# Kernel optimization log

Hardware: AMD Instinct MI355X
Metric: run time of the kernel (lower is better)

The kernel has to match this reference:

```python
import jax, jax.numpy as jnp
import numpy as np
from jax import lax

B, S, T, H, VIN, VOUT = 32, 128, 64, 512, 32000, 32000
PAD_IDX = 1


def setup_inputs() -> dict:
    key = jax.random.key(0)
    ks = jax.random.split(key, 20)
    sc = 0.05
    rn = lambda k, shp: (jax.random.normal(k, shp, jnp.float32) * sc)
    return {
        "src": jax.random.randint(ks[0], (B, S), 0, VIN),
        "src_len": jnp.full((B,), S, dtype=jnp.int32),
        "trg": jax.random.randint(ks[1], (B, T), 0, VOUT),
        "enc_emb": rn(ks[2], (VIN, H)),
        "enc_wih": rn(ks[3], (4 * H, H)),
        "enc_whh": rn(ks[4], (4 * H, H)),
        "enc_bih": rn(ks[5], (4 * H,)),
        "enc_bhh": rn(ks[6], (4 * H,)),
        "enc_fc_w": rn(ks[7], (H, H)),
        "enc_fc_b": rn(ks[8], (H,)),
        "dec_emb": rn(ks[9], (VOUT, H)),
        "attn_w": rn(ks[10], (H, 2 * H)),
        "attn_b": rn(ks[11], (H,)),
        "attn_v": rn(ks[12], (H,)),
        "dec_wih": rn(ks[13], (4 * H, 2 * H)),
        "dec_whh": rn(ks[14], (4 * H, H)),
        "dec_bih": rn(ks[15], (4 * H,)),
        "dec_bhh": rn(ks[16], (4 * H,)),
        "out_w": rn(ks[17], (VOUT, 3 * H)),
        "out_b": rn(ks[18], (VOUT,)),
    }


def _lstm_cell(x, h, c, wih, whh, bih, bhh):
    # PyTorch gate order: i, f, g, o
    g = x @ wih.T + bih + h @ whh.T + bhh
    i, f, gg, o = jnp.split(g, 4, axis=-1)
    c = jax.nn.sigmoid(f) * c + jax.nn.sigmoid(i) * jnp.tanh(gg)
    h = jax.nn.sigmoid(o) * jnp.tanh(c)
    return h, c


def reference(src, src_len, trg, enc_emb, enc_wih, enc_whh, enc_bih, enc_bhh,
              enc_fc_w, enc_fc_b, dec_emb, attn_w, attn_b, attn_v,
              dec_wih, dec_whh, dec_bih, dec_bhh, out_w, out_b):
    b = src.shape[0]
    # ---- Encoder: single-layer LSTM over time (full lengths) ----
    emb = enc_emb[src].transpose(1, 0, 2)  # [S,B,H] time-major
    h0 = jnp.zeros((b, H), emb.dtype)
    c0 = jnp.zeros((b, H), emb.dtype)

    def enc_step(carry, x_t):
        h, c = carry
        h, c = _lstm_cell(x_t, h, c, enc_wih, enc_whh, enc_bih, enc_bhh)
        return (h, c), h

    (hf, cf), enc_out = lax.scan(enc_step, (h0, c0), emb)  # enc_out [S,B,H]
    hidden = jnp.tanh(hf @ enc_fc_w.T + enc_fc_b)  # [B,H]
    enc_bt = enc_out.transpose(1, 0, 2)  # [B,S,H]
    mask = src != PAD_IDX  # [B,S]

    # ---- Decoder: teacher forcing (ratio=1.0), scan over target steps ----
    def dec_step(carry, tok):
        h, c = carry
        e = dec_emb[tok]  # [B,H]
        # Bahdanau attention
        hrep = jnp.broadcast_to(h[:, None, :], enc_bt.shape)  # [B,S,H]
        energy = jnp.tanh(jnp.concatenate([hrep, enc_bt], -1) @ attn_w.T + attn_b)
        score = energy @ attn_v  # [B,S]
        score = jnp.where(mask, score, jnp.float32(-1e10))
        a = jax.nn.softmax(score, axis=1)
        weighted = jnp.einsum('bs,bsh->bh', a, enc_bt)  # [B,H]
        x = jnp.concatenate([e, weighted], -1)  # [B,2H]
        h, c = _lstm_cell(x, h, c, dec_wih, dec_whh, dec_bih, dec_bhh)
        pred = jnp.concatenate([h, weighted, e], -1) @ out_w.T + out_b  # [B,V]
        return (h, c), pred

    tokens = trg.T  # [T,B]
    (_, _), logits = lax.scan(dec_step, (hidden, cf), tokens[:-1])  # [T-1,B,V]
    outputs = jnp.concatenate(
        [jnp.zeros((1, b, VOUT), logits.dtype), logits], axis=0)  # [T,B,V]
    return outputs
```

## Files before the change

### kernel.cpp

```cpp
#include <hip/hip_runtime.h>

typedef unsigned short u16;
typedef unsigned int u32;
typedef unsigned long long u64;
typedef __attribute__((ext_vector_type(8))) short bf16x8;
typedef __attribute__((ext_vector_type(8))) unsigned short u16x8;
typedef __attribute__((ext_vector_type(4))) unsigned short u16x4;
typedef __attribute__((ext_vector_type(4))) float f32x4;

#define DEVI static __device__ __forceinline__

constexpr int B = 32, S = 128, T = 64, H = 512, V = 32000;
constexpr int H4 = 4 * H;
constexpr int TD = T - 1;
constexpr int MOUT = TD * B;
constexpr int KOUT = 3 * H;
constexpr int PAD_IDX = 1;

DEVI u16 f2bf(float f) {
  union { float f; unsigned u; } v; v.f = f;
  unsigned r = (v.u + 0x7fffu + ((v.u >> 16) & 1u)) >> 16;
  return (u16)r;
}
DEVI float bf2f(u16 h) {
  union { unsigned u; float f; } v; v.u = ((unsigned)h) << 16;
  return v.f;
}
DEVI float sigm(float x) { return 1.f / (1.f + __expf(-x)); }
DEVI float tanh_(float x) {
  float ax = fabsf(x);
  float e = __expf(-2.f * ax);
  float t = (1.f - e) / (1.f + e);
  return x < 0.f ? -t : t;
}
DEVI float tanhf_(float x) {
  float e = __expf(2.f * x);
  return 1.f - 2.f * __builtin_amdgcn_rcpf(e + 1.f);
}
DEVI int swz(int row, int k8) { return row * 32 + ((k8 ^ (row & 3)) << 3); }

DEVI u64 pack4u(const u16* p) {
  return (u64)p[0] | ((u64)p[1] << 16) | ((u64)p[2] << 32) | ((u64)p[3] << 48);
}
DEVI u64 xstore(u16* p, u64 v) {
  return __hip_atomic_exchange((u64*)p, v, __ATOMIC_RELAXED,
                               __HIP_MEMORY_SCOPE_AGENT);
}
DEVI void sstore(unsigned* p, unsigned v) {
  __hip_atomic_exchange(p, v, __ATOMIC_RELAXED, __HIP_MEMORY_SCOPE_AGENT);
}
DEVI void poll_slot(unsigned* p, unsigned tgt) {
  long long t0 = (long long)__builtin_amdgcn_s_memrealtime();
  while (__hip_atomic_load(p, __ATOMIC_RELAXED, __HIP_MEMORY_SCOPE_AGENT) <
         tgt) {
    __builtin_amdgcn_s_sleep(1);
    if ((long long)__builtin_amdgcn_s_memrealtime() - t0 > 20000000ll) break;
  }
}

__global__ __launch_bounds__(256) void gemm_bt(
    const u16* __restrict__ A, int lda,
    const u16* __restrict__ Bt, int ldb,
    float* __restrict__ C, int ldc,
    const float* __restrict__ bias, int M, int K, int bf16out) {
  __shared__ u16 As[128 * 32], Bs[128 * 32];
  const int tid = threadIdx.x;
  const int m0 = blockIdx.y * 128, n0 = blockIdx.x * 128;
  const int lane = tid & 63, w = tid >> 6, wm = w >> 1, wn = w & 1;
  const int lr = lane & 15, lk = lane >> 4;
  f32x4 acc[4][4] = {};
  const int r = tid >> 1, cc = (tid & 1) * 16, k8b = (tid & 1) * 2;

  for (int k0 = 0; k0 < K; k0 += 32) {
    {
      long gr = m0 + r;
      u16x8 v0 = {}, v1 = {};
      if (gr < M) {
        const u16* s = A + gr * (long)lda + k0 + cc;
        v0 = *(const u16x8*)s;
        v1 = *(const u16x8*)(s + 8);
      }
      *(u16x8*)&As[swz(r, k8b)] = v0;
      *(u16x8*)&As[swz(r, k8b + 1)] = v1;
    }
    {
      const u16* s = Bt + (long)(n0 + r) * ldb + k0 + cc;
      u16x8 v0 = *(const u16x8*)s;
      u16x8 v1 = *(const u16x8*)(s + 8);
      *(u16x8*)&Bs[swz(r, k8b)] = v0;
      *(u16x8*)&Bs[swz(r, k8b + 1)] = v1;
    }
    __syncthreads();
    bf16x8 af[4], bfr[4];
#pragma unroll
    for (int mi = 0; mi < 4; mi++)
      af[mi] = *(const bf16x8*)&As[swz(wm * 64 + mi * 16 + lr, lk)];
#pragma unroll
    for (int ni = 0; ni < 4; ni++)
      bfr[ni] = *(const bf16x8*)&Bs[swz(wn * 64 + ni * 16 + lr, lk)];
#pragma unroll
    for (int mi = 0; mi < 4; mi++)
#pragma unroll
      for (int ni = 0; ni < 4; ni++)
        acc[mi][ni] = __builtin_amdgcn_mfma_f32_16x16x32_bf16(
            af[mi], bfr[ni], acc[mi][ni], 0, 0, 0);
    __syncthreads();
  }
#pragma unroll
  for (int ni = 0; ni < 4; ni++) {
    int col = n0 + wn * 64 + ni * 16 + lr;
    float bs = bias ? bias[col] : 0.f;
#pragma unroll
    for (int mi = 0; mi < 4; mi++) {
#pragma unroll
      for (int rr = 0; rr < 4; rr++) {
        long row = m0 + wm * 64 + mi * 16 + lk * 4 + rr;
        if (row < M) {
          float v = acc[mi][ni][rr] + bs;
          if (bf16out)
            ((u16*)C)[row * (long)ldc + col] = f2bf(v);
          else
            C[row * (long)ldc + col] = v;
        }
      }
    }
  }
}

__global__ void zero_f(float* p, long n) {
  long i = (long)blockIdx.x * 256 + threadIdx.x;
  long st = (long)gridDim.x * 256;
  for (; i < n; i += st) p[i] = 0.f;
}

__global__ void zero_u(unsigned* p, int n) {
  int i = blockIdx.x * 256 + threadIdx.x;
  if (i < n) p[i] = 0u;
}

__global__ void cast_bf(const float* __restrict__ src, u16* __restrict__ dst,
                        int ld, int off, int Csz) {
  long row = blockIdx.y;
  int col = blockIdx.x * 256 + threadIdx.x;
  dst[row * Csz + col] = f2bf(src[row * ld + off + col]);
}

__global__ void cast_bf4(const float* __restrict__ src, u16* __restrict__ dst,
                         long n4) {
  long i = (long)blockIdx.x * 256 + threadIdx.x;
  if (i >= n4) return;
  float4 v = ((const float4*)src)[i];
  u16x4 o;
  o[0] = f2bf(v.x); o[1] = f2bf(v.y); o[2] = f2bf(v.z); o[3] = f2bf(v.w);
  *(u16x4*)&dst[i * 4] = o;
}

__global__ void cast_perm(const float* __restrict__ src, int ld, int off,
                          u16* __restrict__ dst) {
  int np = blockIdx.y;
  int c = blockIdx.x * 256 + threadIdx.x;
  int g = np & 3, jH = np >> 2;
  dst[(size_t)np * H + c] = f2bf(src[(size_t)(g * H + jH) * ld + off + c]);
}

__global__ void bias_perm(const float* __restrict__ a,
                          const float* __restrict__ b, float* __restrict__ o) {
  int np = blockIdx.x * 256 + threadIdx.x;
  int g = np & 3, jH = np >> 2;
  int r = g * H + jH;
  o[np] = a[r] + b[r];
}

__global__ __launch_bounds__(256) void cast_transpose_bf(
    const float* __restrict__ src, int ld, int off, u16* __restrict__ dst,
    int R) {
  __shared__ float tile[32][33];
  int r0 = blockIdx.y * 32, c0 = blockIdx.x * 32;
  int tx = threadIdx.x & 31, ty = threadIdx.x >> 5;
#pragma unroll
  for (int i = 0; i < 32; i += 8)
    tile[ty + i][tx] = src[(long)(r0 + ty + i) * ld + off + c0 + tx];
  __syncthreads();
#pragma unroll
  for (int i = 0; i < 32; i += 8)
    dst[(long)(c0 + ty + i) * R + r0 + tx] = f2bf(tile[tx][ty + i]);
}

__global__ void gather_src_emb(const int* __restrict__ src,
                               const float* __restrict__ emb,
                               u16* __restrict__ dst) {
  int row = blockIdx.y;
  int t = row >> 5, b = row & 31;
  int c = blockIdx.x * 256 + threadIdx.x;
  int tok = src[b * S + t];
  dst[(long)row * H + c] = f2bf(emb[(long)tok * H + c]);
}

__global__ void gather_trg_emb(const int* __restrict__ trg,
                               const float* __restrict__ emb,
                               u16* __restrict__ xout) {
  int row = blockIdx.y;
  int t = row >> 5, b = row & 31;
  int c = blockIdx.x * 256 + threadIdx.x;
  int tok = trg[b * T + t];
  xout[(long)row * KOUT + 2 * H + c] = f2bf(emb[(long)tok * H + c]);
}

__global__ __launch_bounds__(128) void enc_persist(
    unsigned* fes, const float* __restrict__ whh,
    const float* __restrict__ xih_p, u16* hstep, u16* enc_bt_bf, float* cbuf) {
  const int tid = threadIdx.x, bk = blockIdx.x;
  const int wave = tid >> 6, lane = tid & 63;
  __shared__ float gs[32][16];
  __shared__ float c_s[128];
  __shared__ u16 hx[128];
  bf16x8 wf[16];
  {
    int n = lane & 15, g = n & 3, q = n >> 2;
    const float* wrow =
        whh + ((size_t)g * H + bk * 4 + q) * H + (lane >> 4) * 8;
#pragma unroll
    for (int kt = 0; kt < 16; kt++) {
      bf16x8 f;
#pragma unroll
      for (int e = 0; e < 8; e++) f[e] = (short)f2bf(wrow[kt * 32 + e]);
      wf[kt] = f;
    }
  }
  c_s[tid] = 0.f;
  for (int t = 0; t < S; t++) {
    if (t > 0) {
      poll_slot(fes + tid * 16, (unsigned)t);
      __syncthreads();
    }
    float4 xv = *(const float4*)(xih_p + ((size_t)t * B + (tid >> 2)) * H4 +
                                 (bk * 4 + (tid & 3)) * 4);
    if (t > 0) {
      const u16* hb = hstep + (size_t)t * B * H +
                      (size_t)(wave * 16 + (lane & 15)) * H + (lane >> 4) * 8;
      f32x4 acc = {};
#pragma unroll
      for (int kt = 0; kt < 16; kt++) {
        bf16x8 a = *(const bf16x8*)(hb + kt * 32);
        acc = __builtin_amdgcn_mfma_f32_16x16x32_bf16(a, wf[kt], acc, 0, 0, 0);
      }
      int n = lane & 15, r0 = (lane >> 4) * 4;
#pragma unroll
      for (int rr = 0; rr < 4; rr++) gs[wave * 16 + r0 + rr][n] = acc[rr];
    } else {
      int n = lane & 15, r0 = (lane >> 4) * 4;
#pragma unroll
      for (int rr = 0; rr < 4; rr++) gs[wave * 16 + r0 + rr][n] = 0.f;
    }
    __syncthreads();
    {
      int b = tid >> 2, q = tid & 3;
      float gi = xv.x + gs[b][q * 4 + 0];
      float gf = xv.y + gs[b][q * 4 + 1];
      float gg = xv.z + gs[b][q * 4 + 2];
      float go = xv.w + gs[b][q * 4 + 3];
      float cn = sigm(gf) * c_s[tid] + sigm(gi) * tanh_(gg);
      c_s[tid] = cn;
      float hn = sigm(go) * tanh_(cn);
      u16 h16 = f2bf(hn);
      hx[tid] = h16;
      enc_bt_bf[((size_t)b * S + t) * H + bk * 4 + q] = h16;
    }
    __syncthreads();
    u64 kp = 0;
    if (tid < 32)
      kp = xstore(hstep + (size_t)(t + 1) * B * H + (size_t)tid * H + bk * 4,
                  pack4u(&hx[tid * 4]));
    if (wave == 0) {
      asm volatile("" :: "v"(kp));
      asm volatile("s_waitcnt vmcnt(0)" ::: "memory");
      if (tid == 0) sstore(fes + bk * 16, (unsigned)(t + 1));
    }
  }
  {
    int b = tid >> 2, q = tid & 3;
    cbuf[b * H + bk * 4 + q] = c_s[tid];
  }
}

__global__ __launch_bounds__(512) void dec_persist(
    unsigned* fhs, unsigned* fws, const float* __restrict__ fc_w,
    const float* __restrict__ fc_b, const float* __restrict__ dec_wih,
    const float* __restrict__ dec_whh, const u16* __restrict__ a1T_bf,
    const float* __restrict__ attn_v, const int* __restrict__ src,
    const u16* __restrict__ hf_bf, const float* __restrict__ cbuf,
    const u16* __restrict__ epart_bf, const u16* __restrict__ enc_bt_bf,
    const float* __restrict__ eih_p, u16* hstep, u16* wstep,
    u16* __restrict__ xout_bf) {
  const int tid = threadIdx.x, bk = blockIdx.x;
  const int wave = tid >> 6, lane = tid & 63;
  __shared__ u16 Ws[16 * 1024];
  __shared__ float wsum[8][H];
  __shared__ float hs[H], hps[H];
  __shared__ float gs4[4][32][16];
  __shared__ float sc[S], red[2];
  __shared__ int smask[S];
  __shared__ float c_s[128];
  __shared__ u16 hx[128];
  for (int idx = tid; idx < 16 * 1024; idx += 512) {
    int n = idx >> 10, k = idx & 1023;
    int g = n & 3, q = n >> 2;
    int grow = g * H + bk * 4 + q;
    float v = (k < 512) ? dec_wih[(size_t)grow * (2 * H) + 512 + k]
                        : dec_whh[(size_t)grow * H + (k - 512)];
    Ws[n * 1024 + (((k >> 3) ^ (n & 7)) << 3) + (k & 7)] = f2bf(v);
  }
  if (tid < 128) c_s[tid] = cbuf[(tid >> 2) * H + bk * 4 + (tid & 3)];
  float av8[8];
  if (bk < 32) {
    if (tid < S) smask[tid] = src[bk * S + tid];
#pragma unroll
    for (int e = 0; e < 8; e++) av8[e] = attn_v[lane * 8 + e];
  }
  if (bk < 32 && wave < 2) {
    int n = lane & 15;
    const u16* hb = hf_bf + (size_t)(wave * 16 + n) * H + (lane >> 4) * 8;
    const float* frow = fc_w + (size_t)(bk * 16 + n) * H + (lane >> 4) * 8;
    f32x4 acc = {};
#pragma unroll
    for (int kt = 0; kt < 16; kt++) {
      bf16x8 a = *(const bf16x8*)(hb + kt * 32);
      bf16x8 bf;
#pragma unroll
      for (int e = 0; e < 8; e++) bf[e] = (short)f2bf(frow[kt * 32 + e]);
      acc = __builtin_amdgcn_mfma_f32_16x16x32_bf16(a, bf, acc, 0, 0, 0);
    }
    float bias = fc_b[bk * 16 + n];
    int r0 = (lane >> 4) * 4;
#pragma unroll
    for (int rr = 0; rr < 4; rr++)
      gs4[0][wave * 16 + r0 + rr][n] = tanh_(acc[rr] + bias);
  }
  __syncthreads();
  if (bk < 32) {
    u64 kp = 0;
    if (tid < 128) {
      int b = tid >> 2, qq = tid & 3;
      u16 w0 = f2bf(gs4[0][b][qq * 4 + 0]);
      u16 w1 = f2bf(gs4[0][b][qq * 4 + 1]);
      u16 w2 = f2bf(gs4[0][b][qq * 4 + 2]);
      u16 w3 = f2bf(gs4[0][b][qq * 4 + 3]);
      u64 val = (u64)w0 | ((u64)w1 << 16) | ((u64)w2 << 32) | ((u64)w3 << 48);
      kp = xstore(hstep + (size_t)b * H + bk * 16 + qq * 4, val);
    }
    if (wave < 2) {
      asm volatile("" :: "v"(kp));
      asm volatile("s_waitcnt vmcnt(0)" ::: "memory");
    }
    __syncthreads();
    if (tid == 0) sstore(fhs + bk * 16, 1u);
  }
  for (int t = 0; t < TD; t++) {
    if (tid < 128)
      poll_slot(fhs + tid * 16, (unsigned)(tid < 32 ? t + 1 : t));
    __syncthreads();
    float4 xv = {};
    if (tid < 128)
      xv = *(const float4*)(eih_p + ((size_t)t * B + (tid >> 2)) * H4 +
                            (bk * 4 + (tid & 3)) * 4);
    if (bk < 32) {
      const int b = bk;
      if (tid < 256) {
        u32 v = ((const u32*)(hstep + (size_t)t * B * H + (size_t)b * H))[tid];
        hs[2 * tid] = bf2f((u16)(v & 0xffff));
        hs[2 * tid + 1] = bf2f((u16)(v >> 16));
      }
      __syncthreads();
      {
        float p[8] = {};
        const int j0 = lane * 8;
#pragma unroll 4
        for (int kk = 0; kk < 64; kk++) {
          int k = wave * 64 + kk;
          float hk = hs[k];
          u16x8 av = *(const u16x8*)&a1T_bf[(size_t)k * H + j0];
#pragma unroll
          for (int e = 0; e < 8; e++) p[e] += hk * bf2f(av[e]);
        }
#pragma unroll
        for (int e = 0; e < 8; e++) wsum[wave][j0 + e] = p[e];
      }
      __syncthreads();
      {
        float s0 = 0.f;
#pragma unroll
        for (int w = 0; w < 8; w++) s0 += wsum[w][tid];
        hps[tid] = s0;
      }
      __syncthreads();
      {
        const int j0 = lane * 8;
        float hp8[8];
#pragma unroll
        for (int e = 0; e < 8; e++) hp8[e] = hps[j0 + e];
        for (int i = 0; i < 16; i++) {
          int s = wave * 16 + i;
          u16x8 ep = *(const u16x8*)&epart_bf[((size_t)b * S + s) * H + j0];
          float a = 0.f;
#pragma unroll
          for (int e = 0; e < 8; e++)
            a += av8[e] * tanhf_(hp8[e] + bf2f(ep[e]));
#pragma unroll
          for (int o = 32; o; o >>= 1) a += __shfl_xor(a, o);
          if (lane == 0) sc[s] = a;
        }
      }
      __syncthreads();
      if (tid < S && smask[tid] == PAD_IDX) sc[tid] = -1e10f;
      __syncthreads();
      if (tid < 64) {
        float v = fmaxf(sc[tid], sc[tid + 64]);
#pragma unroll
        for (int o = 32; o; o >>= 1) v = fmaxf(v, __shfl_xor(v, o));
        if (tid == 0) red[0] = v;
      }
      __syncthreads();
      float mx = red[0];
      if (tid < S) sc[tid] = __expf(sc[tid] - mx);
      __syncthreads();
      if (tid < 64) {
        float v = sc[tid] + sc[tid + 64];
#pragma unroll
        for (int o = 32; o; o >>= 1) v += __shfl_xor(v, o);
        if (tid == 0) red[1] = 1.f / v;
      }
      {
        float acc8[8] = {};
        const int j0 = lane * 8;
        for (int i = 0; i < 16; i++) {
          int s = wave * 16 + i;
          float pscale = sc[s];
          u16x8 ev = *(const u16x8*)&enc_bt_bf[((size_t)b * S + s) * H + j0];
#pragma unroll
          for (int e = 0; e < 8; e++) acc8[e] += pscale * bf2f(ev[e]);
        }
#pragma unroll
        for (int e = 0; e < 8; e++) wsum[wave][j0 + e] = acc8[e];
      }
      __syncthreads();
      {
        u64 kp = 0;
        if (tid < 128) {
          float inv = red[1];
          int j0 = tid * 4;
          u16x4 o;
#pragma unroll
          for (int i = 0; i < 4; i++) {
            float wj = (wsum[0][j0 + i] + wsum[1][j0 + i] + wsum[2][j0 + i] +
                        wsum[3][j0 + i] + wsum[4][j0 + i] + wsum[5][j0 + i] +
                        wsum[6][j0 + i] + wsum[7][j0 + i]) *
                       inv;
            o[i] = f2bf(wj);
          }
          *(u16x4*)&xout_bf[((size_t)t * B + b) * KOUT + H + j0] = o;
          u64 val = (u64)o[0] | ((u64)o[1] << 16) | ((u64)o[2] << 32) |
                    ((u64)o[3] << 48);
          kp = xstore(wstep + (size_t)t * B * H + (size_t)b * H + j0, val);
        }
        if (wave < 2) {
          asm volatile("" :: "v"(kp));
          asm volatile("s_waitcnt vmcnt(0)" ::: "memory");
        }
        __syncthreads();
        if (tid == 0) sstore(fws + bk * 16, (unsigned)(t + 1));
      }
    }
    if (wave < 4) {
      int p = wave >> 1, sub = wave & 1;
      int m = lane & 15, ks = lane >> 4;
      const u16* hb =
          hstep + (size_t)t * B * H + (size_t)(sub * 16 + m) * H + ks * 8;
      f32x4 acc = {};
#pragma unroll
      for (int kt = p * 8; kt < p * 8 + 8; kt++) {
        bf16x8 a = *(const bf16x8*)(hb + kt * 32);
        bf16x8 w = *(const bf16x8*)&Ws[m * 1024 +
                                       (((64 + kt * 4 + ks) ^ (m & 7)) << 3)];
        acc = __builtin_amdgcn_mfma_f32_16x16x32_bf16(a, w, acc, 0, 0, 0);
      }
      int r0 = ks * 4;
#pragma unroll
      for (int rr = 0; rr < 4; rr++) gs4[p][sub * 16 + r0 + rr][m] = acc[rr];
    }
    if (tid < 32) poll_slot(fws + tid * 16, (unsigned)(t + 1));
    __syncthreads();
    if (wave >= 4) {
      int w2 = wave - 4, p = w2 >> 1, sub = w2 & 1;
      int m = lane & 15, ks = lane >> 4;
      const u16* wb_ =
          wstep + (size_t)t * B * H + (size_t)(sub * 16 + m) * H + ks * 8;
      f32x4 acc = {};
#pragma unroll
      for (int kt = p * 8; kt < p * 8 + 8; kt++) {
        bf16x8 a = *(const bf16x8*)(wb_ + kt * 32);
        bf16x8 w =
            *(const bf16x8*)&Ws[m * 1024 + (((kt * 4 + ks) ^ (m & 7)) << 3)];
        acc = __builtin_amdgcn_mfma_f32_16x16x32_bf16(a, w, acc, 0, 0, 0);
      }
      int r0 = ks * 4;
#pragma unroll
      for (int rr = 0; rr < 4; rr++)
        gs4[2 + p][sub * 16 + r0 + rr][m] = acc[rr];
    }
    __syncthreads();
    if (tid < 128) {
      int b2 = tid >> 2, q = tid & 3;
      float gi = xv.x + gs4[0][b2][q * 4 + 0] + gs4[1][b2][q * 4 + 0] +
                 gs4[2][b2][q * 4 + 0] + gs4[3][b2][q * 4 + 0];
      float gf = xv.y + gs4[0][b2][q * 4 + 1] + gs4[1][b2][q * 4 + 1] +
                 gs4[2][b2][q * 4 + 1] + gs4[3][b2][q * 4 + 1];
      float gg = xv.z + gs4[0][b2][q * 4 + 2] + gs4[1][b2][q * 4 + 2] +
                 gs4[2][b2][q * 4 + 2] + gs4[3][b2][q * 4 + 2];
      float go = xv.w + gs4[0][b2][q * 4 + 3] + gs4[1][b2][q * 4 + 3] +
                 gs4[2][b2][q * 4 + 3] + gs4[3][b2][q * 4 + 3];
      float cn = sigm(gf) * c_s[tid] + sigm(gi) * tanh_(gg);
      c_s[tid] = cn;
      float hn = sigm(go) * tanh_(cn);
      u16 h16 = f2bf(hn);
      hx[tid] = h16;
      xout_bf[((size_t)t * B + b2) * KOUT + bk * 4 + q] = h16;
    }
    __syncthreads();
    u64 kp2 = 0;
    if (tid < 32)
      kp2 = xstore(hstep + (size_t)(t + 1) * B * H + (size_t)tid * H + bk * 4,
                   pack4u(&hx[tid * 4]));
    if (wave == 0) {
      asm volatile("" :: "v"(kp2));
      asm volatile("s_waitcnt vmcnt(0)" ::: "memory");
      if (tid == 0)
        sstore(fhs + bk * 16, (unsigned)(bk < 32 ? t + 2 : t + 1));
    }
  }
}

extern "C" void kernel_launch(void* const* d_in, const int* in_sizes, int n_in,
                              void* d_out, int out_size, void* d_ws,
                              size_t ws_size, hipStream_t stream) {
  const int* src = (const int*)d_in[0];
  const int* trg = (const int*)d_in[2];
  const float* enc_emb = (const float*)d_in[3];
  const float* enc_wih = (const float*)d_in[4];
  const float* enc_whh = (const float*)d_in[5];
  const float* enc_bih = (const float*)d_in[6];
  const float* enc_bhh = (const float*)d_in[7];
  const float* fc_w = (const float*)d_in[8];
  const float* fc_b = (const float*)d_in[9];
  const float* dec_emb = (const float*)d_in[10];
  const float* attn_w = (const float*)d_in[11];
  const float* attn_b = (const float*)d_in[12];
  const float* attn_v = (const float*)d_in[13];
  const float* dec_wih = (const float*)d_in[14];
  const float* dec_whh = (const float*)d_in[15];
  const float* dec_bih = (const float*)d_in[16];
  const float* dec_bhh = (const float*)d_in[17];
  const float* out_w = (const float*)d_in[18];
  const float* out_b = (const float*)d_in[19];
  float* out = (float*)d_out;

  char* wp = (char*)d_ws;
  auto alloc = [&](size_t n) {
    char* p = wp;
    wp += (n + 255) & ~(size_t)255;
    return p;
  };
  u16* outw_bf = (u16*)alloc((size_t)V * KOUT * 2);
  u16* wihenc_p = (u16*)alloc((size_t)H4 * H * 2);
  u16* wihE_p = (u16*)alloc((size_t)H4 * H * 2);
  u16* attnw2_bf = (u16*)alloc((size_t)H * H * 2);
  u16* a1T_bf = (u16*)alloc((size_t)H * H * 2);
  u16* xemb_bf = (u16*)alloc((size_t)S * B * H * 2);
  float* xih_p = (float*)alloc((size_t)S * B * H4 * 4);
  u16* enc_bt_bf = (u16*)alloc((size_t)B * S * H * 2);
  u16* epart_bf = (u16*)alloc((size_t)B * S * H * 2);
  float* eih_p = (float*)alloc((size_t)MOUT * H4 * 4);
  u16* xout_bf = (u16*)alloc((size_t)MOUT * KOUT * 2);
  u16* hstep_enc = (u16*)alloc((size_t)(S + 1) * B * H * 2);
  u16* hstep_dec = (u16*)alloc((size_t)T * B * H * 2);
  u16* wstep = (u16*)alloc((size_t)TD * B * H * 2);
  float* cbuf = (float*)alloc((size_t)B * H * 4);
  float* benc_p = (float*)alloc((size_t)H4 * 4);
  float* bdec_p = (float*)alloc((size_t)H4 * 4);
  unsigned* flags = (unsigned*)alloc(4608 * 4);
  unsigned* fes = flags;
  unsigned* fhs = flags + 2048;
  unsigned* fws = flags + 4096;

  dim3 blk(256);
  zero_f<<<dim3(256), blk, 0, stream>>>(out, (long)B * V);
  zero_u<<<dim3(18), blk, 0, stream>>>(flags, 4608);
  cast_bf4<<<dim3(((long)V * KOUT / 4 + 255) / 256), blk, 0, stream>>>(
      out_w, outw_bf, (long)V * KOUT / 4);
  cast_perm<<<dim3(H / 256, H4), blk, 0, stream>>>(enc_wih, H, 0, wihenc_p);
  cast_perm<<<dim3(H / 256, H4), blk, 0, stream>>>(dec_wih, 2 * H, 0, wihE_p);
  cast_bf<<<dim3(H / 256, H), blk, 0, stream>>>(attn_w, attnw2_bf, 2 * H, H, H);
  cast_transpose_bf<<<dim3(H / 32, H / 32), blk, 0, stream>>>(attn_w, 2 * H, 0,
                                                              a1T_bf, H);
  bias_perm<<<dim3(H4 / 256), blk, 0, stream>>>(enc_bih, enc_bhh, benc_p);
  bias_perm<<<dim3(H4 / 256), blk, 0, stream>>>(dec_bih, dec_bhh, bdec_p);
  gather_src_emb<<<dim3(H / 256, S * B), blk, 0, stream>>>(src, enc_emb,
                                                           xemb_bf);
  gather_trg_emb<<<dim3(H / 256, MOUT), blk, 0, stream>>>(trg, dec_emb,
                                                          xout_bf);
  gemm_bt<<<dim3(H4 / 128, (S * B) / 128), blk, 0, stream>>>(
      xemb_bf, H, wihenc_p, H, xih_p, H4, benc_p, S * B, H, 0);
  gemm_bt<<<dim3(H4 / 128, (MOUT + 127) / 128), blk, 0, stream>>>(
      xout_bf + 2 * H, KOUT, wihE_p, H, eih_p, H4, bdec_p, MOUT, H, 0);
  enc_persist<<<dim3(128), dim3(128), 0, stream>>>(fes, enc_whh, xih_p,
                                                   hstep_enc, enc_bt_bf, cbuf);
  gemm_bt<<<dim3(H / 128, (B * S) / 128), blk, 0, stream>>>(
      enc_bt_bf, H, attnw2_bf, H, (float*)epart_bf, H, attn_b, B * S, H, 1);
  dec_persist<<<dim3(128), dim3(512), 0, stream>>>(
      fhs, fws, fc_w, fc_b, dec_wih, dec_whh, a1T_bf, attn_v, src,
      hstep_enc + (size_t)S * B * H, cbuf, epart_bf, enc_bt_bf, eih_p,
      hstep_dec, wstep, xout_bf);
  gemm_bt<<<dim3(V / 128, (MOUT + 127) / 128), blk, 0, stream>>>(
      xout_bf, KOUT, outw_bf, KOUT, out + (size_t)B * V, V, out_b, MOUT, KOUT,
      0);
}
```

Measured before the change: 2.623 ms.

## Precompute encoder-output times W_ih so decoder exchanges attention probabilities instead of context

Context times W_ih_w is rewritten as attention-probs times (enc_out times W_ih_w). A new GEMM precomputes G3 = enc_bt times the context half of dec_wih, written in a per-block permuted layout. Each decoder step then publishes only the 128 softmax probabilities per batch row, not the 512-wide weighted context, and every block gathers them to form its gate contribution as a small dot product. This shrinks the cross-block exchange and removes the dependency on all blocks finishing the weighted sum. It costs an extra 32x128x2048 GEMM plus streaming G3 reads each step, and polling now backs off with longer sleeps.

Result: slower. 3.522 ms (+34.3%).

```diff
diff --git a/kernel.cpp b/kernel.cpp
--- a/kernel.cpp
+++ b/kernel.cpp
@@ -9,6 +9,7 @@
 typedef __attribute__((ext_vector_type(4))) float f32x4;
 
 #define DEVI static __device__ __forceinline__
+#define MFMA __builtin_amdgcn_mfma_f32_16x16x32_bf16
 
 constexpr int B = 32, S = 128, T = 64, H = 512, V = 32000;
 constexpr int H4 = 4 * H;
@@ -49,11 +50,17 @@
 DEVI void sstore(unsigned* p, unsigned v) {
   __hip_atomic_exchange(p, v, __ATOMIC_RELAXED, __HIP_MEMORY_SCOPE_AGENT);
 }
-DEVI void poll_slot(unsigned* p, unsigned tgt) {
+DEVI void poll_bo(unsigned* p, unsigned tgt) {
+  int it = 0;
   long long t0 = (long long)__builtin_amdgcn_s_memrealtime();
   while (__hip_atomic_load(p, __ATOMIC_RELAXED, __HIP_MEMORY_SCOPE_AGENT) <
          tgt) {
-    __builtin_amdgcn_s_sleep(1);
+    if (it < 4) {
+      __builtin_amdgcn_s_sleep(1);
+      it++;
+    } else {
+      __builtin_amdgcn_s_sleep(8);
+    }
     if ((long long)__builtin_amdgcn_s_memrealtime() - t0 > 20000000ll) break;
   }
 }
@@ -62,7 +69,7 @@
     const u16* __restrict__ A, int lda,
     const u16* __restrict__ Bt, int ldb,
     float* __restrict__ C, int ldc,
-    const float* __restrict__ bias, int M, int K, int bf16out) {
+    const float* __restrict__ bias, int M, int K, int outmode) {
   __shared__ u16 As[128 * 32], Bs[128 * 32];
   const int tid = threadIdx.x;
   const int m0 = blockIdx.y * 128, n0 = blockIdx.x * 128;
@@ -102,8 +109,7 @@
     for (int mi = 0; mi < 4; mi++)
 #pragma unroll
       for (int ni = 0; ni < 4; ni++)
-        acc[mi][ni] = __builtin_amdgcn_mfma_f32_16x16x32_bf16(
-            af[mi], bfr[ni], acc[mi][ni], 0, 0, 0);
+        acc[mi][ni] = MFMA(af[mi], bfr[ni], acc[mi][ni], 0, 0, 0);
     __syncthreads();
   }
 #pragma unroll
@@ -117,10 +123,16 @@
         long row = m0 + wm * 64 + mi * 16 + lk * 4 + rr;
         if (row < M) {
           float v = acc[mi][ni][rr] + bs;
-          if (bf16out)
+          if (outmode == 0) {
+            C[row * (long)ldc + col] = v;
+          } else if (outmode == 1) {
             ((u16*)C)[row * (long)ldc + col] = f2bf(v);
-          else
-            C[row * (long)ldc + col] = v;
+          } else {
+            int g = col >> 9, jj = col & 511, bkx = jj >> 2, q = jj & 3;
+            int rq = q * 4 + g;
+            long b = row >> 7, s = row & 127;
+            ((u16*)C)[((((size_t)bkx * 32 + b) * 16 + rq) << 7) + s] = f2bf(v);
+          }
         }
       }
     }
@@ -230,7 +242,7 @@
   c_s[tid] = 0.f;
   for (int t = 0; t < S; t++) {
     if (t > 0) {
-      poll_slot(fes + tid * 16, (unsigned)t);
+      poll_bo(fes + tid * 16, (unsigned)t);
       __syncthreads();
     }
     float4 xv = *(const float4*)(xih_p + ((size_t)t * B + (tid >> 2)) * H4 +
@@ -242,7 +254,7 @@
 #pragma unroll
       for (int kt = 0; kt < 16; kt++) {
         bf16x8 a = *(const bf16x8*)(hb + kt * 32);
-        acc = __builtin_amdgcn_mfma_f32_16x16x32_bf16(a, wf[kt], acc, 0, 0, 0);
+        acc = MFMA(a, wf[kt], acc, 0, 0, 0);
       }
       int n = lane & 15, r0 = (lane >> 4) * 4;
 #pragma unroll
@@ -285,30 +297,32 @@
 
 __global__ __launch_bounds__(512) void dec_persist(
     unsigned* fhs, unsigned* fws, const float* __restrict__ fc_w,
-    const float* __restrict__ fc_b, const float* __restrict__ dec_wih,
-    const float* __restrict__ dec_whh, const u16* __restrict__ a1T_bf,
-    const float* __restrict__ attn_v, const int* __restrict__ src,
-    const u16* __restrict__ hf_bf, const float* __restrict__ cbuf,
-    const u16* __restrict__ epart_bf, const u16* __restrict__ enc_bt_bf,
-    const float* __restrict__ eih_p, u16* hstep, u16* wstep,
+    const float* __restrict__ fc_b, const float* __restrict__ dec_whh,
+    const u16* __restrict__ a1T_bf, const float* __restrict__ attn_v,
+    const int* __restrict__ src, const u16* __restrict__ hf_bf,
+    const float* __restrict__ cbuf, const u16* __restrict__ epart_bf,
+    const u16* __restrict__ enc_bt_bf, const u16* __restrict__ G3,
+    const float* __restrict__ eih_p, u16* hstep, u16* pst,
     u16* __restrict__ xout_bf) {
   const int tid = threadIdx.x, bk = blockIdx.x;
   const int wave = tid >> 6, lane = tid & 63;
-  __shared__ u16 Ws[16 * 1024];
+  __shared__ u16 Ws[16 * 512];
   __shared__ float wsum[8][H];
   __shared__ float hs[H], hps[H];
-  __shared__ float gs4[4][32][16];
+  __shared__ float gs4[2][32][16];
+  __shared__ float gsw[32][16];
+  __shared__ u16 ps_s[32][128];
+  __shared__ u16 p_l[128];
   __shared__ float sc[S], red[2];
   __shared__ int smask[S];
   __shared__ float c_s[128];
   __shared__ u16 hx[128];
-  for (int idx = tid; idx < 16 * 1024; idx += 512) {
-    int n = idx >> 10, k = idx & 1023;
+  for (int idx = tid; idx < 16 * 512; idx += 512) {
+    int n = idx >> 9, k = idx & 511;
     int g = n & 3, q = n >> 2;
     int grow = g * H + bk * 4 + q;
-    float v = (k < 512) ? dec_wih[(size_t)grow * (2 * H) + 512 + k]
-                        : dec_whh[(size_t)grow * H + (k - 512)];
-    Ws[n * 1024 + (((k >> 3) ^ (n & 7)) << 3) + (k & 7)] = f2bf(v);
+    Ws[n * 512 + (((k >> 3) ^ (n & 7)) << 3) + (k & 7)] =
+        f2bf(dec_whh[(size_t)grow * H + k]);
   }
   if (tid < 128) c_s[tid] = cbuf[(tid >> 2) * H + bk * 4 + (tid & 3)];
   float av8[8];
@@ -328,7 +342,7 @@
       bf16x8 bf;
 #pragma unroll
       for (int e = 0; e < 8; e++) bf[e] = (short)f2bf(frow[kt * 32 + e]);
-      acc = __builtin_amdgcn_mfma_f32_16x16x32_bf16(a, bf, acc, 0, 0, 0);
+      acc = MFMA(a, bf, acc, 0, 0, 0);
     }
     float bias = fc_b[bk * 16 + n];
     int r0 = (lane >> 4) * 4;
@@ -357,7 +371,7 @@
   }
   for (int t = 0; t < TD; t++) {
     if (tid < 128)
-      poll_slot(fhs + tid * 16, (unsigned)(tid < 32 ? t + 1 : t));
+      poll_bo(fhs + tid * 16, (unsigned)(tid < 32 ? t + 1 : t));
     __syncthreads();
     float4 xv = {};
     if (tid < 128)
@@ -429,6 +443,20 @@
         for (int o = 32; o; o >>= 1) v += __shfl_xor(v, o);
         if (tid == 0) red[1] = 1.f / v;
       }
+      __syncthreads();
+      if (tid < 128) p_l[tid] = f2bf(sc[tid] * red[1]);
+      __syncthreads();
+      {
+        u64 kp = 0;
+        if (tid < 32)
+          kp = xstore(pst + ((size_t)t * B + b) * 128 + tid * 4,
+                      pack4u(&p_l[tid * 4]));
+        if (wave == 0) {
+          asm volatile("" :: "v"(kp));
+          asm volatile("s_waitcnt vmcnt(0)" ::: "memory");
+          if (tid == 0) sstore(fws + bk * 16, (unsigned)(t + 1));
+        }
+      }
       {
         float acc8[8] = {};
         const int j0 = lane * 8;
@@ -443,31 +471,19 @@
         for (int e = 0; e < 8; e++) wsum[wave][j0 + e] = acc8[e];
       }
       __syncthreads();
-      {
-        u64 kp = 0;
-        if (tid < 128) {
-          float inv = red[1];
-          int j0 = tid * 4;
-          u16x4 o;
-#pragma unroll
-          for (int i = 0; i < 4; i++) {
-            float wj = (wsum[0][j0 + i] + wsum[1][j0 + i] + wsum[2][j0 + i] +
-                        wsum[3][j0 + i] + wsum[4][j0 + i] + wsum[5][j0 + i] +
-                        wsum[6][j0 + i] + wsum[7][j0 + i]) *
-                       inv;
-            o[i] = f2bf(wj);
-          }
-          *(u16x4*)&xout_bf[((size_t)t * B + b) * KOUT + H + j0] = o;
-          u64 val = (u64)o[0] | ((u64)o[1] << 16) | ((u64)o[2] << 32) |
-                    ((u64)o[3] << 48);
-          kp = xstore(wstep + (size_t)t * B * H + (size_t)b * H + j0, val);
+      if (tid < 128) {
+        float inv = red[1];
+        int j0 = tid * 4;
+        u16x4 o;
+#pragma unroll
+        for (int i = 0; i < 4; i++) {
+          float wj = (wsum[0][j0 + i] + wsum[1][j0 + i] + wsum[2][j0 + i] +
+                      wsum[3][j0 + i] + wsum[4][j0 + i] + wsum[5][j0 + i] +
+                      wsum[6][j0 + i] + wsum[7][j0 + i]) *
+                     inv;
+          o[i] = f2bf(wj);
         }
-        if (wave < 2) {
-          asm volatile("" :: "v"(kp));
-          asm volatile("s_waitcnt vmcnt(0)" ::: "memory");
-        }
-        __syncthreads();
-        if (tid == 0) sstore(fws + bk * 16, (unsigned)(t + 1));
+        *(u16x4*)&xout_bf[((size_t)t * B + b) * KOUT + H + j0] = o;
       }
     }
     if (wave < 4) {
@@ -479,45 +495,49 @@
 #pragma unroll
       for (int kt = p * 8; kt < p * 8 + 8; kt++) {
         bf16x8 a = *(const bf16x8*)(hb + kt * 32);
-        bf16x8 w = *(const bf16x8*)&Ws[m * 1024 +
-                                       (((64 + kt * 4 + ks) ^ (m & 7)) << 3)];
-        acc = __builtin_amdgcn_mfma_f32_16x16x32_bf16(a, w, acc, 0, 0, 0);
+        bf16x8 w =
+            *(const bf16x8*)&Ws[m * 512 + (((kt * 4 + ks) ^ (m & 7)) << 3)];
+        acc = MFMA(a, w, acc, 0, 0, 0);
       }
       int r0 = ks * 4;
 #pragma unroll
       for (int rr = 0; rr < 4; rr++) gs4[p][sub * 16 + r0 + rr][m] = acc[rr];
-    }
-    if (tid < 32) poll_slot(fws + tid * 16, (unsigned)(t + 1));
-    __syncthreads();
-    if (wave >= 4) {
-      int w2 = wave - 4, p = w2 >> 1, sub = w2 & 1;
-      int m = lane & 15, ks = lane >> 4;
-      const u16* wb_ =
-          wstep + (size_t)t * B * H + (size_t)(sub * 16 + m) * H + ks * 8;
-      f32x4 acc = {};
-#pragma unroll
-      for (int kt = p * 8; kt < p * 8 + 8; kt++) {
-        bf16x8 a = *(const bf16x8*)(wb_ + kt * 32);
-        bf16x8 w =
-            *(const bf16x8*)&Ws[m * 1024 + (((kt * 4 + ks) ^ (m & 7)) << 3)];
-        acc = __builtin_amdgcn_mfma_f32_16x16x32_bf16(a, w, acc, 0, 0, 0);
-      }
-      int r0 = ks * 4;
-#pragma unroll
-      for (int rr = 0; rr < 4; rr++)
-        gs4[2 + p][sub * 16 + r0 + rr][m] = acc[rr];
+    } else {
+      int i = tid - 256;
+      int b = i >> 3, chunk = i & 7;
+      poll_bo(fws + b * 16, (unsigned)(t + 1));
+      const u16* pp = pst + ((size_t)t * B + b) * 128 + chunk * 16;
+      u16x8 v0 = *(const u16x8*)pp;
+      u16x8 v1 = *(const u16x8*)(pp + 8);
+      *(u16x8*)&ps_s[b][chunk * 16] = v0;
+      *(u16x8*)&ps_s[b][chunk * 16 + 8] = v1;
+    }
+    __syncthreads();
+    {
+      int b = tid >> 4, rq = tid & 15;
+      const u16* gp = G3 + ((((size_t)bk * 32 + b) * 16 + rq) << 7);
+      float acc = 0.f;
+#pragma unroll
+      for (int k8 = 0; k8 < 16; k8++) {
+        u16x8 g8 = *(const u16x8*)(gp + k8 * 8);
+        u16x8 pp = *(const u16x8*)&ps_s[b][k8 * 8];
+#pragma unroll
+        for (int e = 0; e < 8; e++)
+          acc = __builtin_fmaf(bf2f(pp[e]), bf2f(g8[e]), acc);
+      }
+      gsw[b][rq] = acc;
     }
     __syncthreads();
     if (tid < 128) {
       int b2 = tid >> 2, q = tid & 3;
       float gi = xv.x + gs4[0][b2][q * 4 + 0] + gs4[1][b2][q * 4 + 0] +
-                 gs4[2][b2][q * 4 + 0] + gs4[3][b2][q * 4 + 0];
+                 gsw[b2][q * 4 + 0];
       float gf = xv.y + gs4[0][b2][q * 4 + 1] + gs4[1][b2][q * 4 + 1] +
-                 gs4[2][b2][q * 4 + 1] + gs4[3][b2][q * 4 + 1];
+                 gsw[b2][q * 4 + 1];
       float gg = xv.z + gs4[0][b2][q * 4 + 2] + gs4[1][b2][q * 4 + 2] +
-                 gs4[2][b2][q * 4 + 2] + gs4[3][b2][q * 4 + 2];
+                 gsw[b2][q * 4 + 2];
       float go = xv.w + gs4[0][b2][q * 4 + 3] + gs4[1][b2][q * 4 + 3] +
-                 gs4[2][b2][q * 4 + 3] + gs4[3][b2][q * 4 + 3];
+                 gsw[b2][q * 4 + 3];
       float cn = sigm(gf) * c_s[tid] + sigm(gi) * tanh_(gg);
       c_s[tid] = cn;
       float hn = sigm(go) * tanh_(cn);
@@ -572,17 +592,19 @@
   u16* outw_bf = (u16*)alloc((size_t)V * KOUT * 2);
   u16* wihenc_p = (u16*)alloc((size_t)H4 * H * 2);
   u16* wihE_p = (u16*)alloc((size_t)H4 * H * 2);
+  u16* wihW_bf = (u16*)alloc((size_t)H4 * H * 2);
   u16* attnw2_bf = (u16*)alloc((size_t)H * H * 2);
   u16* a1T_bf = (u16*)alloc((size_t)H * H * 2);
   u16* xemb_bf = (u16*)alloc((size_t)S * B * H * 2);
   float* xih_p = (float*)alloc((size_t)S * B * H4 * 4);
   u16* enc_bt_bf = (u16*)alloc((size_t)B * S * H * 2);
   u16* epart_bf = (u16*)alloc((size_t)B * S * H * 2);
+  u16* G3 = (u16*)alloc((size_t)B * S * H4 * 2);
   float* eih_p = (float*)alloc((size_t)MOUT * H4 * 4);
   u16* xout_bf = (u16*)alloc((size_t)MOUT * KOUT * 2);
   u16* hstep_enc = (u16*)alloc((size_t)(S + 1) * B * H * 2);
   u16* hstep_dec = (u16*)alloc((size_t)T * B * H * 2);
-  u16* wstep = (u16*)alloc((size_t)TD * B * H * 2);
+  u16* pst = (u16*)alloc((size_t)TD * B * 128 * 2);
   float* cbuf = (float*)alloc((size_t)B * H * 4);
   float* benc_p = (float*)alloc((size_t)H4 * 4);
   float* bdec_p = (float*)alloc((size_t)H4 * 4);
@@ -598,6 +620,7 @@
       out_w, outw_bf, (long)V * KOUT / 4);
   cast_perm<<<dim3(H / 256, H4), blk, 0, stream>>>(enc_wih, H, 0, wihenc_p);
   cast_perm<<<dim3(H / 256, H4), blk, 0, stream>>>(dec_wih, 2 * H, 0, wihE_p);
+  cast_bf<<<dim3(H / 256, H4), blk, 0, stream>>>(dec_wih, wihW_bf, 2 * H, H, H);
   cast_bf<<<dim3(H / 256, H), blk, 0, stream>>>(attn_w, attnw2_bf, 2 * H, H, H);
   cast_transpose_bf<<<dim3(H / 32, H / 32), blk, 0, stream>>>(attn_w, 2 * H, 0,
                                                               a1T_bf, H);
@@ -615,10 +638,12 @@
                                                    hstep_enc, enc_bt_bf, cbuf);
   gemm_bt<<<dim3(H / 128, (B * S) / 128), blk, 0, stream>>>(
       enc_bt_bf, H, attnw2_bf, H, (float*)epart_bf, H, attn_b, B * S, H, 1);
+  gemm_bt<<<dim3(H4 / 128, (B * S) / 128), blk, 0, stream>>>(
+      enc_bt_bf, H, wihW_bf, H, (float*)G3, H4, nullptr, B * S, H, 2);
   dec_persist<<<dim3(128), dim3(512), 0, stream>>>(
-      fhs, fws, fc_w, fc_b, dec_wih, dec_whh, a1T_bf, attn_v, src,
-      hstep_enc + (size_t)S * B * H, cbuf, epart_bf, enc_bt_bf, eih_p,
-      hstep_dec, wstep, xout_bf);
+      fhs, fws, fc_w, fc_b, dec_whh, a1T_bf, attn_v, src,
+      hstep_enc + (size_t)S * B * H, cbuf, epart_bf, enc_bt_bf, G3, eih_p,
+      hstep_dec, pst, xout_bf);
   gemm_bt<<<dim3(V / 128, (MOUT + 127) / 128), blk, 0, stream>>>(
       xout_bf, KOUT, outw_bf, KOUT, out + (size_t)B * V, V, out_b, MOUT, KOUT,
       0);
```
